# Kernel optimization log

Measured on AMD Instinct MI355X. Metric: run time of the kernel, lower is better.

The kernel has to match this reference:

```python
import jax, jax.numpy as jnp
import numpy as np

N, E, G = 32768, 262144, 512
IN_DIM, HID, HEADS = 300, 128, 4
D_FUSED = HID * HEADS  # 512
L = 3


def setup_inputs() -> dict:
    key = jax.random.key(0)
    ks = jax.random.split(key, 24)
    s = 0.02
    inp = {
        "x": jax.random.normal(ks[0], (N, IN_DIM), jnp.float32),
        "edge_index": jax.random.randint(ks[1], (2, E), 0, N, jnp.int32),
        "batch": jnp.sort(jax.random.randint(ks[2], (N,), 0, G, jnp.int32)),
        "syn_w": jax.random.normal(ks[3], (IN_DIM, HID)) * s,
        "syn_b": jnp.zeros((HID,), jnp.float32),
        "ant_w": jax.random.normal(ks[4], (IN_DIM, HID)) * s,
        "ant_b": jnp.zeros((HID,), jnp.float32),
        "fusion_w": jax.random.normal(ks[5], (2 * HID, D_FUSED)) * s,
        "fusion_b": jnp.zeros((D_FUSED,), jnp.float32),
        "Wq": jax.random.normal(ks[6], (L, D_FUSED, D_FUSED)) * s,
        "bq": jnp.zeros((L, D_FUSED), jnp.float32),
        "Wk": jax.random.normal(ks[7], (L, D_FUSED, D_FUSED)) * s,
        "bk": jnp.zeros((L, D_FUSED), jnp.float32),
        "Wv": jax.random.normal(ks[8], (L, D_FUSED, D_FUSED)) * s,
        "bv": jnp.zeros((L, D_FUSED), jnp.float32),
        "Wskip": jax.random.normal(ks[9], (L, D_FUSED, D_FUSED)) * s,
        "bskip": jnp.zeros((L, D_FUSED), jnp.float32),
        "cls_w1": jax.random.normal(ks[10], (D_FUSED, HID)) * s,
        "cls_b1": jnp.zeros((HID,), jnp.float32),
        "cls_w2": jax.random.normal(ks[11], (HID, 1)) * s,
        "cls_b2": jnp.zeros((1,), jnp.float32),
    }
    return inp


def _transformer_conv(h, src, dst, Wq, bq, Wk, bk, Wv, bv, Wskip, bskip):
    # PyG TransformerConv: per-edge dot-product attention, softmax over in-neighbors of dst,
    # concat heads, plus root/skip linear (root_weight=True, concat=True, no edge_attr).
    n = h.shape[0]
    q = (h @ Wq + bq).reshape(n, HEADS, HID)
    k = (h @ Wk + bk).reshape(n, HEADS, HID)
    v = (h @ Wv + bv).reshape(n, HEADS, HID)
    scale = 1.0 / np.sqrt(HID)
    logits = jnp.einsum("ehd,ehd->eh", q[dst], k[src]) * scale  # [E, H]
    m = jax.ops.segment_max(logits, dst, num_segments=n)        # [N, H]
    e = jnp.exp(logits - m[dst])
    z = jax.ops.segment_sum(e, dst, num_segments=n)
    alpha = e / (z[dst] + 1e-16)                                # [E, H]
    msg = alpha[:, :, None] * v[src]                            # [E, H, D]
    out = jax.ops.segment_sum(msg, dst, num_segments=n).reshape(n, D_FUSED)
    return out + h @ Wskip + bskip


def reference(x, edge_index, batch, syn_w, syn_b, ant_w, ant_b, fusion_w, fusion_b,
              Wq, bq, Wk, bk, Wv, bv, Wskip, bskip, cls_w1, cls_b1, cls_w2, cls_b2):
    x_syn = jax.nn.relu(x @ syn_w + syn_b)
    x_ant = jax.nn.relu(x @ ant_w + ant_b)
    h = jnp.concatenate([x_syn, x_ant], axis=1) @ fusion_w + fusion_b  # [N, 512]
    src, dst = edge_index[0], edge_index[1]
    for l in range(L):
        h = jax.nn.relu(_transformer_conv(h, src, dst, Wq[l], bq[l], Wk[l], bk[l],
                                          Wv[l], bv[l], Wskip[l], bskip[l]))
    cnt = jax.ops.segment_sum(jnp.ones((h.shape[0],), h.dtype), batch, num_segments=G)
    pooled = jax.ops.segment_sum(h, batch, num_segments=G) / jnp.maximum(cnt, 1.0)[:, None]
    hid = jax.nn.relu(pooled @ cls_w1 + cls_b1)
    out = jax.nn.sigmoid(hid @ cls_w2 + cls_b2)
    return out.squeeze()
```

## Files before the change

### kernel.cpp

```cpp
#include <hip/hip_runtime.h>
#include <hip/hip_bf16.h>
#include <math.h>

#define N_NODES 32768
#define N_EDGES 262144
#define N_GRAPHS 512
#define IN_DIM 300
#define KPAD 320
#define HID 128
#define HEADS 4
#define D_FUSED 512
#define N_LAYERS 3

typedef __hip_bfloat16 bf16;
typedef short bf16x8 __attribute__((ext_vector_type(8)));
typedef float f32x4 __attribute__((ext_vector_type(4)));

__device__ __forceinline__ float bfs_to_f(short s)
{
    unsigned u = ((unsigned)(unsigned short)s) << 16;
    return __builtin_bit_cast(float, u);
}

__device__ __forceinline__ short f_to_bfs(float v)
{
    return (short)__builtin_bit_cast(unsigned short, __float2bfloat16(v));
}

__device__ __forceinline__ void bf8_to_f32(bf16x8 v, float* f)
{
#pragma unroll
    for (int j = 0; j < 8; ++j) f[j] = bfs_to_f(v[j]);
}

__device__ __forceinline__ void gload_lds16(const void* g, void* l)
{
    __builtin_amdgcn_global_load_lds(
        (const __attribute__((address_space(1))) void*)g,
        (__attribute__((address_space(3))) void*)l, 16, 0, 0);
}

template <int ACT>
__global__ __launch_bounds__(512, 2) void mfma_gemm256(
    const bf16* __restrict__ A, int lda,
    const bf16* __restrict__ Bt,
    const float* __restrict__ bias,
    bf16* __restrict__ C0, int ldc0,
    bf16* __restrict__ C1, int ldc1, int csplit,
    int K, int nbx)
{
    __shared__ __align__(16) char lds[131072];

    const int t = threadIdx.x;
    const int wid = t >> 6, lane = t & 63;
    const int hi = lane >> 4, li = lane & 15;
    const int wr = wid >> 2, wc = wid & 3;

    int wg = blockIdx.x;
    if ((gridDim.x & 7) == 0) {
        const int cpx = gridDim.x >> 3;
        wg = (wg & 7) * cpx + (wg >> 3);
    }
    const int mb = wg / nbx, nb = wg % nbx;
    const int brow = mb * 256, bcol = nb * 256;
    const int NT = K >> 6;

    const bf16* gA[4];
    const bf16* gB[4];
    int lbA[4], lbB[4];
#pragma unroll
    for (int j = 0; j < 4; ++j) {
        const int c = j * 512 + wid * 64 + lane;
        const int row = c >> 3;
        const int colb8 = ((c & 7) ^ (row & 7)) * 8;
        gA[j] = A + (size_t)(brow + row) * lda + colb8;
        gB[j] = Bt + (size_t)(bcol + row) * K + colb8;
        lbA[j] = (j * 512 + wid * 64) * 16;
        lbB[j] = 32768 + (j * 512 + wid * 64) * 16;
    }

    f32x4 acc[8][4] = {};

    auto stage = [&](int buf, int kt) {
        const int ko = kt * 64;
#pragma unroll
        for (int j = 0; j < 4; ++j)
            gload_lds16(gA[j] + ko, lds + buf * 65536 + lbA[j]);
#pragma unroll
        for (int j = 0; j < 4; ++j)
            gload_lds16(gB[j] + ko, lds + buf * 65536 + lbB[j]);
    };

    auto compute = [&](int b) {
        const char* Ab = lds + b * 65536;
        const char* Bb = Ab + 32768;
        bf16x8 bfrag[4][2];
#pragma unroll
        for (int n = 0; n < 4; ++n)
#pragma unroll
            for (int ks = 0; ks < 2; ++ks) {
                const int row = wc * 64 + n * 16 + li;
                bfrag[n][ks] = *(const bf16x8*)(
                    Bb + row * 128 + (((ks * 4 + hi) ^ (row & 7)) << 4));
            }
#pragma unroll
        for (int p = 0; p < 4; ++p) {
            bf16x8 afrag[2][2];
#pragma unroll
            for (int mm = 0; mm < 2; ++mm)
#pragma unroll
                for (int ks = 0; ks < 2; ++ks) {
                    const int row = wr * 128 + (p * 2 + mm) * 16 + li;
                    afrag[mm][ks] = *(const bf16x8*)(
                        Ab + row * 128 + (((ks * 4 + hi) ^ (row & 7)) << 4));
                }
            __builtin_amdgcn_s_setprio(1);
#pragma unroll
            for (int mm = 0; mm < 2; ++mm)
#pragma unroll
                for (int n = 0; n < 4; ++n)
#pragma unroll
                    for (int ks = 0; ks < 2; ++ks)
                        acc[p * 2 + mm][n] = __builtin_amdgcn_mfma_f32_16x16x32_bf16(
                            afrag[mm][ks], bfrag[n][ks], acc[p * 2 + mm][n], 0, 0, 0);
            __builtin_amdgcn_s_setprio(0);
        }
    };

    stage(0, 0);
    for (int kt = 0; kt < NT - 1; ++kt) {
        const int b = kt & 1;
        stage(b ^ 1, kt + 1);
        asm volatile("s_waitcnt vmcnt(8)" ::: "memory");
        __builtin_amdgcn_s_barrier();
        compute(b);
        asm volatile("" ::: "memory");
        __builtin_amdgcn_s_barrier();
    }
    asm volatile("s_waitcnt vmcnt(0)" ::: "memory");
    __builtin_amdgcn_s_barrier();
    compute((NT - 1) & 1);

#pragma unroll
    for (int m = 0; m < 8; ++m) {
#pragma unroll
        for (int n = 0; n < 4; ++n) {
            const int col = bcol + wc * 64 + n * 16 + li;
            const float bv = bias[col];
            const bool lo = (col < csplit);
            bf16* Cd = lo ? C0 : C1;
            const int ldc = lo ? ldc0 : ldc1;
            const int cc = lo ? col : col - csplit;
#pragma unroll
            for (int r = 0; r < 4; ++r) {
                const int row = brow + wr * 128 + m * 16 + hi * 4 + r;
                float v = acc[m][n][r] + bv;
                if (ACT == 1) v = fmaxf(v, 0.f);
                Cd[(size_t)row * ldc + cc] = __float2bfloat16(v);
            }
        }
    }
}

template <int ACT>
__global__ __launch_bounds__(256) void mfma_gemm(
    const bf16* __restrict__ A, int lda,
    const bf16* __restrict__ Bt,
    const float* __restrict__ bias,
    bf16* __restrict__ C, int ldc, int K)
{
    __shared__ __align__(16) char lds[16384];
    char* As = lds;
    char* Bs = lds + 8192;

    const int t = threadIdx.x;
    const int wid = t >> 6, lane = t & 63;
    const int brow = blockIdx.x * 128;
    const int bcol = blockIdx.y * 128;
    const int wr = wid >> 1, wc = wid & 1;

    f32x4 acc[4][4] = {};

    for (int k0 = 0; k0 < K; k0 += 32) {
#pragma unroll
        for (int j = 0; j < 2; ++j) {
            const int seg = wid * 2 + j;
            const int row = seg * 16 + (lane >> 2);
            const int clin = lane & 3;
            const int clog = clin ^ ((row >> 1) & 3);
            gload_lds16(A + (size_t)(brow + row) * lda + k0 + clog * 8,
                        As + seg * 1024);
            gload_lds16(Bt + (size_t)(bcol + row) * K + k0 + clog * 8,
                        Bs + seg * 1024);
        }
        __syncthreads();

        bf16x8 af[4], bfr[4];
#pragma unroll
        for (int m = 0; m < 4; ++m) {
            const int row = wr * 64 + m * 16 + (lane & 15);
            const int cl = (lane >> 4) ^ ((row >> 1) & 3);
            af[m] = *(const bf16x8*)(As + row * 64 + cl * 16);
        }
#pragma unroll
        for (int n = 0; n < 4; ++n) {
            const int row = wc * 64 + n * 16 + (lane & 15);
            const int cl = (lane >> 4) ^ ((row >> 1) & 3);
            bfr[n] = *(const bf16x8*)(Bs + row * 64 + cl * 16);
        }
#pragma unroll
        for (int m = 0; m < 4; ++m)
#pragma unroll
            for (int n = 0; n < 4; ++n)
                acc[m][n] = __builtin_amdgcn_mfma_f32_16x16x32_bf16(
                    af[m], bfr[n], acc[m][n], 0, 0, 0);
        __syncthreads();
    }

#pragma unroll
    for (int m = 0; m < 4; ++m) {
#pragma unroll
        for (int n = 0; n < 4; ++n) {
            const int col = bcol + wc * 64 + n * 16 + (lane & 15);
            const float bv = bias[col];
#pragma unroll
            for (int r = 0; r < 4; ++r) {
                const int row = brow + wr * 64 + m * 16 + (lane >> 4) * 4 + r;
                float v = acc[m][n][r] + bv;
                if (ACT == 1) v = fmaxf(v, 0.f);
                C[(size_t)row * ldc + col] = __float2bfloat16(v);
            }
        }
    }
}

__global__ void prep_xpad_kernel(const float* __restrict__ x, bf16* __restrict__ xb)
{
    const int n = blockIdx.x, k = threadIdx.x;
    xb[(size_t)n * KPAD + k] =
        __float2bfloat16(k < IN_DIM ? x[(size_t)n * IN_DIM + k] : 0.f);
}

__global__ void prep_encw_kernel(const float* __restrict__ syn_w,
                                 const float* __restrict__ ant_w,
                                 bf16* __restrict__ wt)
{
    const int c = blockIdx.x, k = threadIdx.x;
    float v = 0.f;
    if (k < IN_DIM) v = (c < HID) ? syn_w[k * HID + c] : ant_w[k * HID + (c - HID)];
    wt[c * KPAD + k] = __float2bfloat16(v);
}

__global__ void prep_fusw_kernel(const float* __restrict__ fw, bf16* __restrict__ wt)
{
    const int c = blockIdx.x, k = threadIdx.x;
    wt[c * 256 + k] = __float2bfloat16(fw[k * D_FUSED + c]);
}

__global__ void prep_combw_kernel(const float* __restrict__ Wskip,
                                  const float* __restrict__ Wq,
                                  const float* __restrict__ Wk,
                                  const float* __restrict__ Wv,
                                  bf16* __restrict__ wt)
{
    const int blk = blockIdx.x;
    const int k = threadIdx.x;
    const int l = blk >> 11, c = blk & 2047;
    float v;
    if (c < 512) {
        v = Wskip[((size_t)l * D_FUSED + k) * D_FUSED + c];
    } else {
        const int cc = c - 512, hd = cc / 384, r = cc % 384;
        const int sel = r >> 7, rr = r & 127;
        const float* s = (sel == 0) ? Wq : (sel == 1) ? Wk : Wv;
        v = s[((size_t)l * D_FUSED + k) * D_FUSED + hd * HID + rr];
    }
    wt[(size_t)blk * D_FUSED + k] = __float2bfloat16(v);
}

__global__ void prep_bias_kernel(const float* __restrict__ syn_b,
                                 const float* __restrict__ ant_b,
                                 const float* __restrict__ bskip,
                                 const float* __restrict__ bq,
                                 const float* __restrict__ bk,
                                 const float* __restrict__ bv,
                                 float* __restrict__ benc,
                                 float* __restrict__ bcomb)
{
    const int i = blockIdx.x * 256 + threadIdx.x;
    if (i < 256) benc[i] = (i < HID) ? syn_b[i] : ant_b[i - HID];
    const int j = i - 256;
    if (j >= 0 && j < 6144) {
        const int l = j >> 11, c = j & 2047;
        float v;
        if (c < 512) {
            v = bskip[l * D_FUSED + c];
        } else {
            const int cc = c - 512, hd = cc / 384, r = cc % 384;
            const int sel = r >> 7, rr = r & 127;
            const float* s = (sel == 0) ? bq : (sel == 1) ? bk : bv;
            v = s[l * D_FUSED + hd * HID + rr];
        }
        bcomb[j] = v;
    }
}

__global__ void zero_int_kernel(int* __restrict__ p, int n)
{
    int i = blockIdx.x * 256 + threadIdx.x;
    if (i < n) p[i] = 0;
}

__global__ void hist_kernel(const int* __restrict__ dst, int* __restrict__ deg, int E)
{
    int e = blockIdx.x * 256 + threadIdx.x;
    if (e < E) atomicAdd(&deg[dst[e]], 1);
}

__global__ __launch_bounds__(256) void partial_sum_kernel(const int* __restrict__ deg,
                                                          int* __restrict__ part)
{
    int v = deg[blockIdx.x * 256 + threadIdx.x];
#pragma unroll
    for (int o = 32; o; o >>= 1) v += __shfl_xor(v, o);
    __shared__ int w4[4];
    if ((threadIdx.x & 63) == 0) w4[threadIdx.x >> 6] = v;
    __syncthreads();
    if (threadIdx.x == 0) part[blockIdx.x] = w4[0] + w4[1] + w4[2] + w4[3];
}

__global__ __launch_bounds__(128) void scan_part_kernel(int* __restrict__ part)
{
    __shared__ int s[128];
    const int t = threadIdx.x;
    s[t] = part[t];
    __syncthreads();
    for (int o = 1; o < 128; o <<= 1) {
        int v = (t >= o) ? s[t - o] : 0;
        __syncthreads();
        s[t] += v;
        __syncthreads();
    }
    part[t] = (t == 0) ? 0 : s[t - 1];
}

__global__ __launch_bounds__(256) void off_kernel(const int* __restrict__ deg,
                                                  const int* __restrict__ part,
                                                  int* __restrict__ off)
{
    __shared__ int s[256];
    const int b = blockIdx.x, t = threadIdx.x;
    s[t] = deg[b * 256 + t];
    __syncthreads();
    for (int o = 1; o < 256; o <<= 1) {
        int v = (t >= o) ? s[t - o] : 0;
        __syncthreads();
        s[t] += v;
        __syncthreads();
    }
    const int excl = (t == 0) ? 0 : s[t - 1];
    off[b * 256 + t] = part[b] + excl;
    if (b == 127 && t == 255) off[N_NODES] = part[127] + s[255];
}

__global__ void scatter_kernel(const int* __restrict__ src, const int* __restrict__ dst,
                               const int* __restrict__ off, int* __restrict__ cursor,
                               int* __restrict__ csr_src, int E)
{
    int e = blockIdx.x * 256 + threadIdx.x;
    if (e < E) {
        int d = dst[e];
        int pos = atomicAdd(&cursor[d], 1);
        csr_src[off[d] + pos] = src[e];
    }
}

__global__ __launch_bounds__(256) void attn_kernel(
    const bf16* __restrict__ qkv, bf16* __restrict__ hout,
    const int* __restrict__ off, const int* __restrict__ csr)
{
    const int n = blockIdx.x;
    const int hd = threadIdx.x >> 6;
    const int lane = threadIdx.x & 63;
    const int g = lane >> 4, sub = lane & 15;
    const float scale = 0.08838834764831845f;

    const bf16* qrow = qkv + (size_t)n * 1536 + hd * 384;
    float qf[8];
    bf8_to_f32(*(const bf16x8*)(qrow + sub * 8), qf);

    float m = -1e30f, z = 0.f;
    float acc[8] = {};

    const int s0 = off[n], s1 = off[n + 1];
    for (int e0 = s0; e0 < s1; e0 += 4) {
        const int e = e0 + g;
        const bool valid = (e < s1);
        const int srcn = valid ? csr[e] : 0;
        const bf16* kp = qkv + (size_t)srcn * 1536 + hd * 384 + 128;

        float kf[8];
        bf8_to_f32(*(const bf16x8*)(kp + sub * 8), kf);
        float d = 0.f;
#pragma unroll
        for (int j = 0; j < 8; ++j) d = fmaf(qf[j], kf[j], d);
        d += __shfl_xor(d, 1);
        d += __shfl_xor(d, 2);
        d += __shfl_xor(d, 4);
        d += __shfl_xor(d, 8);

        const float logit = d * scale;
        const float mn = valid ? fmaxf(m, logit) : m;
        const float corr = __expf(m - mn);
        const float w = valid ? __expf(logit - mn) : 0.f;
        z = z * corr + w;

        float vf[8];
        bf8_to_f32(*(const bf16x8*)(kp + 128 + sub * 8), vf);
#pragma unroll
        for (int j = 0; j < 8; ++j) acc[j] = acc[j] * corr + w * vf[j];
        m = mn;
    }

    float mm = fmaxf(m, __shfl_xor(m, 16));
    mm = fmaxf(mm, __shfl_xor(mm, 32));
    const float f = __expf(m - mm);
    float zz = z * f;
    zz += __shfl_xor(zz, 16);
    zz += __shfl_xor(zz, 32);
    const float inv = 1.f / (zz + 1e-16f);

    float o[8];
#pragma unroll
    for (int j = 0; j < 8; ++j) {
        float a = acc[j] * f;
        a += __shfl_xor(a, 16);
        a += __shfl_xor(a, 32);
        o[j] = a * inv;
    }

    if (g == 0) {
        const size_t ob = (size_t)n * D_FUSED + hd * HID + sub * 8;
        const bf16x8 sk = *(const bf16x8*)(hout + ob);
        bf16x8 res;
#pragma unroll
        for (int j = 0; j < 8; ++j)
            res[j] = f_to_bfs(fmaxf(o[j] + bfs_to_f(sk[j]), 0.f));
        *(bf16x8*)(hout + ob) = res;
    }
}

__global__ __launch_bounds__(256) void pool_kernel(const bf16* __restrict__ h,
                                                   const int* __restrict__ batch,
                                                   float* __restrict__ pooled)
{
    const int g = blockIdx.x;
    int a = 0, b = N_NODES;
    while (a < b) { int mid = (a + b) >> 1; if (batch[mid] < g) a = mid + 1; else b = mid; }
    const int start = a;
    b = N_NODES;
    while (a < b) { int mid = (a + b) >> 1; if (batch[mid] < g + 1) a = mid + 1; else b = mid; }
    const int end = a;
    const float invc = 1.f / fmaxf((float)(end - start), 1.f);

    const int t = threadIdx.x;
    float2 s = make_float2(0.f, 0.f);
    for (int nidx = start; nidx < end; ++nidx) {
        const bf16* p = h + (size_t)nidx * D_FUSED + t * 2;
        s.x += bfs_to_f(((const short*)p)[0]);
        s.y += bfs_to_f(((const short*)p)[1]);
    }
    pooled[(size_t)g * D_FUSED + t * 2]     = s.x * invc;
    pooled[(size_t)g * D_FUSED + t * 2 + 1] = s.y * invc;
}

__global__ __launch_bounds__(128) void cls_kernel(const float* __restrict__ pooled,
                                                  const float* __restrict__ w1,
                                                  const float* __restrict__ b1,
                                                  const float* __restrict__ w2,
                                                  const float* __restrict__ b2,
                                                  float* __restrict__ out)
{
    const int g = blockIdx.x;
    const int j = threadIdx.x;
    const float* p = pooled + (size_t)g * D_FUSED;
    float acc = 0.f;
    for (int i = 0; i < D_FUSED; ++i) acc += p[i] * w1[i * HID + j];
    const float hid = fmaxf(acc + b1[j], 0.f);
    float val = hid * w2[j];
#pragma unroll
    for (int o = 32; o; o >>= 1) val += __shfl_xor(val, o);
    __shared__ float ws2[2];
    if ((threadIdx.x & 63) == 0) ws2[threadIdx.x >> 6] = val;
    __syncthreads();
    if (threadIdx.x == 0) {
        const float sum = ws2[0] + ws2[1] + b2[0];
        out[g] = 1.f / (1.f + __expf(-sum));
    }
}

extern "C" void kernel_launch(void* const* d_in, const int* in_sizes, int n_in,
                              void* d_out, int out_size, void* d_ws, size_t ws_size,
                              hipStream_t stream)
{
    const float* x        = (const float*)d_in[0];
    const int*   ei       = (const int*)d_in[1];
    const int*   batch    = (const int*)d_in[2];
    const float* syn_w    = (const float*)d_in[3];
    const float* syn_b    = (const float*)d_in[4];
    const float* ant_w    = (const float*)d_in[5];
    const float* ant_b    = (const float*)d_in[6];
    const float* fusion_w = (const float*)d_in[7];
    const float* fusion_b = (const float*)d_in[8];
    const float* Wq       = (const float*)d_in[9];
    const float* bq       = (const float*)d_in[10];
    const float* Wk       = (const float*)d_in[11];
    const float* bk       = (const float*)d_in[12];
    const float* Wv       = (const float*)d_in[13];
    const float* bv       = (const float*)d_in[14];
    const float* Wskip    = (const float*)d_in[15];
    const float* bskip    = (const float*)d_in[16];
    const float* cls_w1   = (const float*)d_in[17];
    const float* cls_b1   = (const float*)d_in[18];
    const float* cls_w2   = (const float*)d_in[19];
    const float* cls_b2   = (const float*)d_in[20];

    const int* src = ei;
    const int* dst = ei + N_EDGES;

    const size_t NV = (size_t)N_NODES * D_FUSED;
    bf16* hA    = (bf16*)d_ws;
    bf16* hB    = hA + NV;
    bf16* qs    = hB + NV;
    bf16* wenc  = qs + (size_t)N_NODES * 1536;
    bf16* wfus  = wenc + 256 * KPAD;
    bf16* wcomb = wfus + 512 * 256;
    float* benc = (float*)(wcomb + (size_t)3 * 2048 * 512);
    float* bcomb = benc + 256;
    float* pooled = bcomb + 6144;
    int* deg    = (int*)(pooled + (size_t)N_GRAPHS * D_FUSED);
    int* cursor = deg + N_NODES;
    int* part   = cursor + N_NODES;
    int* off    = part + 128;
    int* csr    = off + N_NODES + 1;

    bf16* xb   = qs;
    bf16* tenc = hB;

    zero_int_kernel<<<(2 * N_NODES + 255) / 256, 256, 0, stream>>>(deg, 2 * N_NODES);
    hist_kernel<<<N_EDGES / 256, 256, 0, stream>>>(dst, deg, N_EDGES);
    partial_sum_kernel<<<128, 256, 0, stream>>>(deg, part);
    scan_part_kernel<<<1, 128, 0, stream>>>(part);
    off_kernel<<<128, 256, 0, stream>>>(deg, part, off);
    scatter_kernel<<<N_EDGES / 256, 256, 0, stream>>>(src, dst, off, cursor, csr, N_EDGES);

    prep_xpad_kernel<<<N_NODES, KPAD, 0, stream>>>(x, xb);
    prep_encw_kernel<<<256, KPAD, 0, stream>>>(syn_w, ant_w, wenc);
    prep_fusw_kernel<<<512, 256, 0, stream>>>(fusion_w, wfus);
    prep_combw_kernel<<<6144, 512, 0, stream>>>(Wskip, Wq, Wk, Wv, wcomb);
    prep_bias_kernel<<<25, 256, 0, stream>>>(syn_b, ant_b, bskip, bq, bk, bv, benc, bcomb);

    mfma_gemm<1><<<dim3(N_NODES / 128, 2), 256, 0, stream>>>(
        xb, KPAD, wenc, benc, tenc, 256, KPAD);
    mfma_gemm256<0><<<256, 512, 0, stream>>>(
        tenc, 256, wfus, fusion_b, hA, D_FUSED, hA, D_FUSED, D_FUSED, 256, 2);

    bf16* hcur = hA;
    bf16* hnew = hB;
    for (int l = 0; l < N_LAYERS; ++l) {
        mfma_gemm256<0><<<1024, 512, 0, stream>>>(
            hcur, D_FUSED, wcomb + (size_t)l * 2048 * D_FUSED,
            bcomb + (size_t)l * 2048,
            hnew, D_FUSED, qs, 1536, 512, D_FUSED, 8);
        attn_kernel<<<N_NODES, 256, 0, stream>>>(qs, hnew, off, csr);
        bf16* tmp = hcur; hcur = hnew; hnew = tmp;
    }

    pool_kernel<<<N_GRAPHS, 256, 0, stream>>>(hcur, batch, pooled);
    cls_kernel<<<N_GRAPHS, 128, 0, stream>>>(pooled, cls_w1, cls_b1, cls_w2, cls_b2,
                                             (float*)d_out);
}
```

Measured before the change: 655.5 us.

## Template GEMM on K, reorder MFMA loops, and tile-transpose combined weight prep

Makes K a compile-time template parameter of the 256x256 MFMA GEMM so the k-tile loop can be fully unrolled, and reorders the MFMA inner loops so the ks dimension is outermost. It also rewrites the combined-weight transpose kernel to use a 32x33 shared-memory tile, so both the fp32 reads and the bf16 writes are coalesced instead of strided. The changes target loop overhead in the GEMMs and uncoalesced access in weight prep, at the cost of larger code size and two template instantiations.

```diff
diff --git a/kernel.cpp b/kernel.cpp
--- a/kernel.cpp
+++ b/kernel.cpp
@@ -40,14 +40,14 @@
         (__attribute__((address_space(3))) void*)l, 16, 0, 0);
 }
 
-template <int ACT>
+template <int K, int ACT>
 __global__ __launch_bounds__(512, 2) void mfma_gemm256(
     const bf16* __restrict__ A, int lda,
     const bf16* __restrict__ Bt,
     const float* __restrict__ bias,
     bf16* __restrict__ C0, int ldc0,
     bf16* __restrict__ C1, int ldc1, int csplit,
-    int K, int nbx)
+    int nbx)
 {
     __shared__ __align__(16) char lds[131072];
 
@@ -63,7 +63,7 @@
     }
     const int mb = wg / nbx, nb = wg % nbx;
     const int brow = mb * 256, bcol = nb * 256;
-    const int NT = K >> 6;
+    constexpr int NT = K >> 6;
 
     const bf16* gA[4];
     const bf16* gB[4];
@@ -116,11 +116,11 @@
                 }
             __builtin_amdgcn_s_setprio(1);
 #pragma unroll
-            for (int mm = 0; mm < 2; ++mm)
-#pragma unroll
-                for (int n = 0; n < 4; ++n)
-#pragma unroll
-                    for (int ks = 0; ks < 2; ++ks)
+            for (int ks = 0; ks < 2; ++ks)
+#pragma unroll
+                for (int mm = 0; mm < 2; ++mm)
+#pragma unroll
+                    for (int n = 0; n < 4; ++n)
                         acc[p * 2 + mm][n] = __builtin_amdgcn_mfma_f32_16x16x32_bf16(
                             afrag[mm][ks], bfrag[n][ks], acc[p * 2 + mm][n], 0, 0, 0);
             __builtin_amdgcn_s_setprio(0);
@@ -128,6 +128,7 @@
     };
 
     stage(0, 0);
+#pragma unroll
     for (int kt = 0; kt < NT - 1; ++kt) {
         const int b = kt & 1;
         stage(b ^ 1, kt + 1);
@@ -257,25 +258,45 @@
     wt[c * 256 + k] = __float2bfloat16(fw[k * D_FUSED + c]);
 }
 
-__global__ void prep_combw_kernel(const float* __restrict__ Wskip,
-                                  const float* __restrict__ Wq,
-                                  const float* __restrict__ Wk,
-                                  const float* __restrict__ Wv,
-                                  bf16* __restrict__ wt)
-{
+__global__ __launch_bounds__(256) void prep_combw_kernel(
+    const float* __restrict__ Wskip,
+    const float* __restrict__ Wq,
+    const float* __restrict__ Wk,
+    const float* __restrict__ Wv,
+    bf16* __restrict__ wt)
+{
+    __shared__ float tile[32][33];
     const int blk = blockIdx.x;
-    const int k = threadIdx.x;
-    const int l = blk >> 11, c = blk & 2047;
-    float v;
-    if (c < 512) {
-        v = Wskip[((size_t)l * D_FUSED + k) * D_FUSED + c];
+    const int l = blk >> 10, rem = blk & 1023;
+    const int cb = rem >> 4, kb = rem & 15;
+    const int c0 = cb * 32;
+
+    const float* mat;
+    int cp0;
+    if (c0 < 512) {
+        mat = Wskip; cp0 = c0;
     } else {
-        const int cc = c - 512, hd = cc / 384, r = cc % 384;
-        const int sel = r >> 7, rr = r & 127;
-        const float* s = (sel == 0) ? Wq : (sel == 1) ? Wk : Wv;
-        v = s[((size_t)l * D_FUSED + k) * D_FUSED + hd * HID + rr];
-    }
-    wt[(size_t)blk * D_FUSED + k] = __float2bfloat16(v);
+        const int cc0 = c0 - 512;
+        const int hd = cc0 / 384, r0 = cc0 % 384;
+        const int sel = r0 >> 7, rr0 = r0 & 127;
+        mat = (sel == 0) ? Wq : (sel == 1) ? Wk : Wv;
+        cp0 = hd * 128 + rr0;
+    }
+
+    const int j = threadIdx.x & 31;
+    const int i0 = threadIdx.x >> 5;
+#pragma unroll
+    for (int s = 0; s < 4; ++s) {
+        const int i = i0 + 8 * s;
+        tile[i][j] = mat[((size_t)l * 512 + kb * 32 + i) * 512 + cp0 + j];
+    }
+    __syncthreads();
+#pragma unroll
+    for (int s = 0; s < 4; ++s) {
+        const int jj = i0 + 8 * s;
+        wt[((size_t)l * 2048 + c0 + jj) * 512 + kb * 32 + j] =
+            __float2bfloat16(tile[j][jj]);
+    }
 }
 
 __global__ void prep_bias_kernel(const float* __restrict__ syn_b,
@@ -557,21 +578,21 @@
     prep_xpad_kernel<<<N_NODES, KPAD, 0, stream>>>(x, xb);
     prep_encw_kernel<<<256, KPAD, 0, stream>>>(syn_w, ant_w, wenc);
     prep_fusw_kernel<<<512, 256, 0, stream>>>(fusion_w, wfus);
-    prep_combw_kernel<<<6144, 512, 0, stream>>>(Wskip, Wq, Wk, Wv, wcomb);
+    prep_combw_kernel<<<3072, 256, 0, stream>>>(Wskip, Wq, Wk, Wv, wcomb);
     prep_bias_kernel<<<25, 256, 0, stream>>>(syn_b, ant_b, bskip, bq, bk, bv, benc, bcomb);
 
     mfma_gemm<1><<<dim3(N_NODES / 128, 2), 256, 0, stream>>>(
         xb, KPAD, wenc, benc, tenc, 256, KPAD);
-    mfma_gemm256<0><<<256, 512, 0, stream>>>(
-        tenc, 256, wfus, fusion_b, hA, D_FUSED, hA, D_FUSED, D_FUSED, 256, 2);
+    mfma_gemm256<256, 0><<<256, 512, 0, stream>>>(
+        tenc, 256, wfus, fusion_b, hA, D_FUSED, hA, D_FUSED, D_FUSED, 2);
 
     bf16* hcur = hA;
     bf16* hnew = hB;
     for (int l = 0; l < N_LAYERS; ++l) {
-        mfma_gemm256<0><<<1024, 512, 0, stream>>>(
+        mfma_gemm256<512, 0><<<1024, 512, 0, stream>>>(
             hcur, D_FUSED, wcomb + (size_t)l * 2048 * D_FUSED,
             bcomb + (size_t)l * 2048,
-            hnew, D_FUSED, qs, 1536, 512, D_FUSED, 8);
+            hnew, D_FUSED, qs, 1536, 512, 8);
         attn_kernel<<<N_NODES, 256, 0, stream>>>(qs, hnew, off, csr);
         bf16* tmp = hcur; hcur = hnew; hnew = tmp;
     }
```

Measured after the change: 635.8 us. 3.0% less time.
